# Kernel optimization log

Hardware: AMD Instinct MI355X
Metric: run time of the kernel (lower is better)

## Reference

```python
import math
import jax, jax.numpy as jnp
import numpy as np

B, T, S, D, H, L, DFF, IN, PERIOD = 16, 600, 600, 1024, 8, 8, 4096, 52, 25
HD = D // H
NEG = -1e9


def _param(key, name, shape, scale=0.02):
    k = jax.random.fold_in(key, hash(name) % (2**31))
    return jax.random.normal(k, shape, dtype=jnp.float32) * scale


def setup_inputs() -> dict:
    key = jax.random.key(0)
    k1, k2, k3 = jax.random.split(key, 3)
    inp = {}
    inp["x"] = jax.random.normal(k1, (B, T, IN), dtype=jnp.float32)
    inp["memory"] = jax.random.normal(k2, (B, S, D), dtype=jnp.float32)
    inp["timesteps"] = jax.random.randint(k3, (B,), 0, 1000, dtype=jnp.int32)

    # Periodic positional encoding buffer: sinusoidal over one period, tiled.
    pos = jnp.arange(PERIOD, dtype=jnp.float32)[:, None]
    div = jnp.exp(jnp.arange(0, D, 2, dtype=jnp.float32) * (-math.log(10000.0) / D))
    pe_p = jnp.zeros((PERIOD, D), dtype=jnp.float32)
    pe_p = pe_p.at[:, 0::2].set(jnp.sin(pos * div)).at[:, 1::2].set(jnp.cos(pos * div))
    inp["pe"] = jnp.tile(pe_p, (T // PERIOD + 1, 1))[:T]  # [T, D]

    # ALiBi-style periodic bias (vectorized form of init_bi_biased_mask_faceformer).
    # alibi[h,i,j] = -slope_h * floor((i-j)/period) for j<=i, -slope_h*floor((j-i-1)/period) for j>i
    slopes = jnp.array([0.5 ** (h + 1) for h in range(H)], dtype=jnp.float32)
    di = jnp.arange(T)[:, None] - jnp.arange(T)[None, :]
    steps = jnp.where(di >= 0, di // PERIOD, (-di - 1) // PERIOD).astype(jnp.float32)
    inp["alibi"] = -slopes[:, None, None] * steps[None]  # [H, T, T]

    # Parameters
    inp["W_in"] = _param(key, "W_in", (D, IN))
    inp["b_in"] = jnp.zeros((D,), jnp.float32)
    inp["te_W1"] = _param(key, "te_W1", (D, D))
    inp["te_b1"] = jnp.zeros((D,), jnp.float32)
    inp["te_W2"] = _param(key, "te_W2", (D, D))
    inp["te_b2"] = jnp.zeros((D,), jnp.float32)
    for nm, shape in [
        ("sa_Wqkv", (L, 3 * D, D)), ("sa_bqkv", (L, 3 * D)),
        ("sa_Wo", (L, D, D)), ("sa_bo", (L, D)),
        ("ca_Wqkv", (L, 3 * D, D)), ("ca_bqkv", (L, 3 * D)),
        ("ca_Wo", (L, D, D)), ("ca_bo", (L, D)),
        ("ff_W1", (L, DFF, D)), ("ff_b1", (L, DFF)),
        ("ff_W2", (L, D, DFF)), ("ff_b2", (L, D)),
    ]:
        inp[nm] = _param(key, nm, shape)
    for nm in ["ln1_g", "ln2_g", "ln3_g"]:
        inp[nm] = jnp.ones((L, D), jnp.float32)
    for nm in ["ln1_b", "ln2_b", "ln3_b"]:
        inp[nm] = jnp.zeros((L, D), jnp.float32)
    inp["W_out"] = _param(key, "W_out", (IN, D))
    inp["b_out"] = jnp.zeros((IN,), jnp.float32)
    return inp


def _ln(x, g, b, eps=1e-5):
    mu = jnp.mean(x, axis=-1, keepdims=True)
    var = jnp.mean(jnp.square(x - mu), axis=-1, keepdims=True)
    return (x - mu) * jax.lax.rsqrt(var + eps) * g + b


def _mha(q_in, kv_in, Wqkv, bqkv, Wo, bo, bias):
    # q_in: [B,Tq,D]; kv_in: [B,Tk,D]; bias broadcastable to [B,H,Tq,Tk]
    Wq, Wk, Wv = jnp.split(Wqkv, 3, axis=0)
    bq, bk, bv = jnp.split(bqkv, 3, axis=0)
    Bn, Tq, _ = q_in.shape
    Tk = kv_in.shape[1]
    q = (q_in @ Wq.T + bq).reshape(Bn, Tq, H, HD).transpose(0, 2, 1, 3)
    k = (kv_in @ Wk.T + bk).reshape(Bn, Tk, H, HD).transpose(0, 2, 1, 3)
    v = (kv_in @ Wv.T + bv).reshape(Bn, Tk, H, HD).transpose(0, 2, 1, 3)
    scores = jnp.einsum("bhqd,bhkd->bhqk", q, k) / math.sqrt(HD) + bias
    attn = jax.nn.softmax(scores, axis=-1)
    out = jnp.einsum("bhqk,bhkd->bhqd", attn, v)
    out = out.transpose(0, 2, 1, 3).reshape(Bn, Tq, D)
    return out @ Wo.T + bo


def reference(x, memory, timesteps, pe, alibi, W_in, b_in, te_W1, te_b1, te_W2, te_b2,
              sa_Wqkv, sa_bqkv, sa_Wo, sa_bo, ca_Wqkv, ca_bqkv, ca_Wo, ca_bo,
              ff_W1, ff_b1, ff_W2, ff_b2, ln1_g, ln1_b, ln2_g, ln2_b, ln3_g, ln3_b,
              W_out, b_out):
    # --- timestep embedding (DDPM sinusoidal + 2-layer SiLU MLP) ---
    half = D // 2
    exponent = jnp.exp(-math.log(10000.0) * jnp.arange(half, dtype=jnp.float32) / (half - 1.0))
    emb = timesteps.astype(jnp.float32)[:, None] * exponent[None, :]
    t_emb = jnp.concatenate([jnp.sin(emb), jnp.cos(emb)], axis=-1)  # [B, D]
    t_emb = jax.nn.silu(t_emb @ te_W1.T + te_b1) @ te_W2.T + te_b2
    adapter = t_emb[:, None, :]  # [B, 1, D] adapter token

    # --- input projection + periodic positional encoding ---
    h = x @ W_in.T + b_in + pe[None]  # [B, T, D]

    # --- attention biases (adapter column is always attendable => zero bias) ---
    sa_bias = jnp.concatenate([jnp.zeros((H, T, 1), jnp.float32), alibi], axis=-1)[None]  # [1,H,T,1+T]
    eye = jnp.eye(T, S, dtype=jnp.float32)
    mem_bias = jnp.where(eye > 0, 0.0, NEG)  # FaceFormer diagonal-only memory mask
    mem_bias = jnp.concatenate([jnp.zeros((T, 1), jnp.float32), mem_bias], axis=-1)[None, None]  # [1,1,T,1+S]

    # --- stacked decoder layers (post-norm, adapter prepended to K/V) ---
    for l in range(L):
        x_adpt = jnp.concatenate([adapter, h], axis=1)  # [B, 1+T, D]
        h = _ln(h + _mha(h, x_adpt, sa_Wqkv[l], sa_bqkv[l], sa_Wo[l], sa_bo[l], sa_bias), ln1_g[l], ln1_b[l])
        mem_adpt = jnp.concatenate([adapter, memory], axis=1)  # [B, 1+S, D]
        h = _ln(h + _mha(h, mem_adpt, ca_Wqkv[l], ca_bqkv[l], ca_Wo[l], ca_bo[l], mem_bias), ln2_g[l], ln2_b[l])
        ff = jax.nn.relu(h @ ff_W1[l].T + ff_b1[l]) @ ff_W2[l].T + ff_b2[l]
        h = _ln(h + ff, ln3_g[l], ln3_b[l])

    return h @ W_out.T + b_out  # [B, T, IN]
```

## Files before the change

kernel.cpp:

```cpp
#include <hip/hip_runtime.h>
#include <stdint.h>

#define B_ 16
#define T_ 600
#define S_ 600
#define D_ 1024
#define H_ 8
#define HD_ 128
#define L_ 8
#define DFF_ 4096
#define IN_ 52
#define TP1 601
#define MTOK 9600
#define MPAD 9728
#define VTK 608

typedef unsigned short u16;
typedef float f32x4 __attribute__((ext_vector_type(4)));
typedef __bf16 bf16x8 __attribute__((ext_vector_type(8)));

__device__ __forceinline__ u16 f2bf(float f){
  union { float f; unsigned u; } v; v.f = f;
  v.u += 0x7FFFu + ((v.u >> 16) & 1u);
  return (u16)(v.u >> 16);
}
__device__ __forceinline__ float bf2f(u16 h){
  union { unsigned u; float f; } v; v.u = ((unsigned)h) << 16;
  return v.f;
}
__device__ __forceinline__ void gld_lds16(const void* g, void* l){
  __builtin_amdgcn_global_load_lds(
      (const __attribute__((address_space(1))) void*)(uintptr_t)g,
      (__attribute__((address_space(3))) void*)(uintptr_t)l, 16, 0, 0);
}
__device__ __forceinline__ f32x4 MM(bf16x8 a, bf16x8 b, f32x4 c){
  return __builtin_amdgcn_mfma_f32_16x16x32_bf16(a, b, c, 0, 0, 0);
}
#define BAR() asm volatile("s_barrier" ::: "memory")

template<int EPI>
__global__ __launch_bounds__(512, 2)
void k_gemm256(const u16* __restrict__ A, const u16* __restrict__ W,
               const float* __restrict__ bias, void* __restrict__ Cout,
               float* __restrict__ hres, int N, int K, int Mstore){
  __shared__ u16 lds[65536];
  const int t = threadIdx.x;
  const int w = t >> 6, l = t & 63;
  const int lr = l & 15, lg = l >> 4;
  const int wr = w >> 2, wc = w & 3;

  int lin = blockIdx.y * gridDim.x + blockIdx.x;
  const int nwg = gridDim.x * gridDim.y;
  lin = (lin & 7) * (nwg >> 3) + (lin >> 3);
  const long m0 = (long)(lin / gridDim.x) * 256;
  const long n0 = (long)(lin % gridDim.x) * 256;

  const int srow = w*8 + (l >> 3);
  const int schk = (l & 7) ^ (l >> 3);
  const u16* gA = A + (m0 + srow) * (long)K + schk * 8;
  const u16* gB = W + (n0 + srow) * (long)K + schk * 8;

  const int chk0 = ((    lg) ^ (lr & 7)) * 8;
  const int chk1 = ((4 + lg) ^ (lr & 7)) * 8;
  const int arow = (wr*128 + lr) * 64;
  const int brow = (wc*64  + lr) * 64 + 16384;

  f32x4 acc[8][4] = {};
  const int NT = K >> 6;

#define STG_A(i) gld_lds16(gA + (long)(i)*64*K + nc, (void*)(lds + nb + (i)*4096 + w*512))
#define STG_B(i) gld_lds16(gB + (long)(i)*64*K + nc, (void*)(lds + nb + 16384 + (i)*4096 + w*512))
#define LOADF(mq, CH) \
    a0 = *(const bf16x8*)(lds + bufo + arow + ((mq)*4+0)*1024 + (CH)); \
    a1 = *(const bf16x8*)(lds + bufo + arow + ((mq)*4+1)*1024 + (CH)); \
    a2 = *(const bf16x8*)(lds + bufo + arow + ((mq)*4+2)*1024 + (CH)); \
    a3 = *(const bf16x8*)(lds + bufo + arow + ((mq)*4+3)*1024 + (CH)); \
    b0 = *(const bf16x8*)(lds + bufo + brow + 0*1024 + (CH)); \
    b1 = *(const bf16x8*)(lds + bufo + brow + 1*1024 + (CH)); \
    b2 = *(const bf16x8*)(lds + bufo + brow + 2*1024 + (CH));  \
    b3 = *(const bf16x8*)(lds + bufo + brow + 3*1024 + (CH));
#define MFMA16(mq) \
    __builtin_amdgcn_s_setprio(1); \
    { const bf16x8 aa[4] = {a0,a1,a2,a3}; const bf16x8 bb4[4] = {b0,b1,b2,b3}; \
      _Pragma("unroll") for (int i_ = 0; i_ < 4; i_++) \
        _Pragma("unroll") for (int j_ = 0; j_ < 4; j_++) \
          acc[(mq)*4+i_][j_] = MM(aa[i_], bb4[j_], acc[(mq)*4+i_][j_]); } \
    __builtin_amdgcn_s_setprio(0);

  { const int nb = 0; const long nc = 0;
    STG_B(0); STG_B(1); STG_B(2); STG_B(3);
    STG_A(0); STG_A(2); STG_A(1); STG_A(3);
  }
  asm volatile("s_waitcnt vmcnt(2)" ::: "memory");
  BAR();

  int bufo = 0;
  for (int tt = 0; tt < NT; ++tt){
    const int nb = bufo ^ 32768;
    const bool st = (tt + 1 < NT);
    const long nc = (long)(tt + 1) * 64;
    bf16x8 a0,a1,a2,a3,b0,b1,b2,b3;
    LOADF(0, chk0);
    if (st){ STG_B(0); STG_B(1); }
    BAR();
    MFMA16(0);
    BAR();
    LOADF(0, chk1);
    if (st){ STG_B(2); STG_B(3); asm volatile("s_waitcnt vmcnt(4)" ::: "memory"); }
    else   {                     asm volatile("s_waitcnt vmcnt(0)" ::: "memory"); }
    BAR();
    MFMA16(0);
    BAR();
    LOADF(1, chk0);
    if (st){ STG_A(0); STG_A(2); }
    BAR();
    MFMA16(1);
    BAR();
    LOADF(1, chk1);
    if (st){ STG_A(1); STG_A(3); asm volatile("s_waitcnt vmcnt(2)" ::: "memory"); }
    BAR();
    MFMA16(1);
    BAR();
    bufo = nb;
  }
#undef STG_A
#undef STG_B
#undef LOADF
#undef MFMA16

  const int r4 = lg * 4;
#pragma unroll
  for (int nf = 0; nf < 4; nf++){
    const long col = n0 + wc*64 + nf*16 + lr;
    const float bv = bias[col];
#pragma unroll
    for (int mf = 0; mf < 8; mf++){
      const long row = m0 + wr*128 + mf*16 + r4;
      if (EPI == 2 && row >= Mstore) continue;
#pragma unroll
      for (int r = 0; r < 4; r++){
        float v = acc[mf][nf][r] + bv;
        if (EPI == 1) v = fmaxf(v, 0.f);
        if (EPI == 2) hres[(row + r) * (long)N + col] += v;
        else          ((u16*)Cout)[(row + r) * (long)N + col] = f2bf(v);
      }
    }
  }
}

template<int EPI>
__global__ __launch_bounds__(512, 4)
void k_gemm_n64(const u16* __restrict__ A, const u16* __restrict__ W,
                const float* __restrict__ bias, void* __restrict__ Cout,
                float* __restrict__ hres, int N, int K, int Mstore){
  __shared__ u16 lds[40960];
  const int t = threadIdx.x;
  const int w = t >> 6, l = t & 63;
  const int lr = l & 15, lg = l >> 4;
  const int wr = w >> 1, wcc = w & 1;

  int lin = blockIdx.y * gridDim.x + blockIdx.x;
  const int nwg = gridDim.x * gridDim.y;
  lin = (lin & 7) * (nwg >> 3) + (lin >> 3);
  const long m0 = (long)(lin / gridDim.x) * 256;
  const long n0 = (long)(lin % gridDim.x) * 64;

  const int srow = w*8 + (l >> 3);
  const int schk = (l & 7) ^ (l >> 3);
  const u16* gA = A + (m0 + srow) * (long)K + schk * 8;
  const u16* gB = W + (n0 + srow) * (long)K + schk * 8;

  const int swz = lr & 7;
  const int arowb = wr*4096 + lr*64;
  const int browb = 16384 + (wcc*32 + lr)*64;

  f32x4 acc[4][2] = {};
  const int NT = K >> 6;

#define STG_A64(i) gld_lds16(gA + (long)(i)*64*K + nc, (void*)(lds + nb + (i)*4096 + w*512))
#define STG_B64()  gld_lds16(gB + nc,                  (void*)(lds + nb + 16384 + w*512))
#define LOADF64(kk) \
    a0 = *(const bf16x8*)(lds + bufo + arowb + 0*1024 + (((kk)*4+lg)^swz)*8); \
    a1 = *(const bf16x8*)(lds + bufo + arowb + 1*1024 + (((kk)*4+lg)^swz)*8); \
    a2 = *(const bf16x8*)(lds + bufo + arowb + 2*1024 + (((kk)*4+lg)^swz)*8); \
    a3 = *(const bf16x8*)(lds + bufo + arowb + 3*1024 + (((kk)*4+lg)^swz)*8); \
    b0 = *(const bf16x8*)(lds + bufo + browb + 0*1024 + (((kk)*4+lg)^swz)*8); \
    b1 = *(const bf16x8*)(lds + bufo + browb + 1*1024 + (((kk)*4+lg)^swz)*8);
#define MFMA8() \
    __builtin_amdgcn_s_setprio(1); \
    { const bf16x8 aa[4] = {a0,a1,a2,a3}; \
      _Pragma("unroll") for (int i_ = 0; i_ < 4; i_++){ \
        acc[i_][0] = MM(aa[i_], b0, acc[i_][0]); \
        acc[i_][1] = MM(aa[i_], b1, acc[i_][1]); } } \
    __builtin_amdgcn_s_setprio(0);

  { const int nb = 0; const long nc = 0;
    STG_B64(); STG_A64(0); STG_A64(1); STG_A64(2); STG_A64(3);
  }
  asm volatile("s_waitcnt vmcnt(0)" ::: "memory");
  BAR();

  int bufo = 0;
  for (int tt = 0; tt < NT; ++tt){
    const int nb = (bufo ^ 20480);
    const bool st = (tt + 1 < NT);
    const long nc = (long)(tt + 1) * 64;
    bf16x8 a0,a1,a2,a3,b0,b1;
    if (st){ STG_B64(); STG_A64(0); STG_A64(1); STG_A64(2); STG_A64(3); }
    LOADF64(0);
    MFMA8();
    LOADF64(1);
    MFMA8();
    if (st) asm volatile("s_waitcnt vmcnt(0)" ::: "memory");
    BAR();
    bufo = nb;
  }
#undef STG_A64
#undef STG_B64
#undef LOADF64
#undef MFMA8

  const int r4 = lg * 4;
#pragma unroll
  for (int nf = 0; nf < 2; nf++){
    const long col = n0 + wcc*32 + nf*16 + lr;
    const float bv = bias[col];
#pragma unroll
    for (int mf = 0; mf < 4; mf++){
      const long row = m0 + wr*64 + mf*16 + r4;
      if (EPI == 2 && row >= Mstore) continue;
#pragma unroll
      for (int r = 0; r < 4; r++){
        float v = acc[mf][nf][r] + bv;
        if (EPI == 1) v = fmaxf(v, 0.f);
        if (EPI == 2) hres[(row + r) * (long)N + col] += v;
        else          ((u16*)Cout)[(row + r) * (long)N + col] = f2bf(v);
      }
    }
  }
}

__global__ __launch_bounds__(256)
void k_gemm_in(const u16* __restrict__ A, const u16* __restrict__ W,
               const float* __restrict__ bias, const float* __restrict__ pe,
               float* __restrict__ hf, u16* __restrict__ hbf){
  __shared__ u16 sA[128*64];
  __shared__ u16 sB[128*64];
  const int t = threadIdx.x;
  const int w = t >> 6, l = t & 63;
  const int lr = l & 15, lg = l >> 4;
  const long m0 = (long)blockIdx.y * 128;
  const long n0 = (long)blockIdx.x * 128;
  const int wm = (w >> 1) << 6, wn = (w & 1) << 6;
  const int srow = t >> 3;
  const int schk = (t & 7) ^ (srow & 7);
  const u16* gA = A + (m0 + srow) * 64 + schk * 8;
  const u16* gB = W + (n0 + srow) * 64 + schk * 8;
#pragma unroll
  for (int i = 0; i < 4; i++){
    gld_lds16(gA + i*32*64, (void*)(sA + i*2048 + (t>>6)*512));
    gld_lds16(gB + i*32*64, (void*)(sB + i*2048 + (t>>6)*512));
  }
  asm volatile("s_waitcnt vmcnt(0)" ::: "memory");
  __syncthreads();
  f32x4 acc[4][4] = {};
#pragma unroll
  for (int kk = 0; kk < 2; kk++){
    bf16x8 af[4], bfv[4];
#pragma unroll
    for (int i = 0; i < 4; i++){
      const int row = wm + i*16 + lr;
      af[i] = *(const bf16x8*)(sA + row*64 + ((kk*4+lg)^(row&7))*8);
    }
#pragma unroll
    for (int j = 0; j < 4; j++){
      const int row = wn + j*16 + lr;
      bfv[j] = *(const bf16x8*)(sB + row*64 + ((kk*4+lg)^(row&7))*8);
    }
#pragma unroll
    for (int i = 0; i < 4; i++)
#pragma unroll
      for (int j = 0; j < 4; j++)
        acc[i][j] = MM(af[i], bfv[j], acc[i][j]);
  }
  const int r0 = lg * 4;
#pragma unroll
  for (int j = 0; j < 4; j++){
    const long col = n0 + wn + j*16 + lr;
    const float bv = bias[col];
#pragma unroll
    for (int i = 0; i < 4; i++){
      const long row = m0 + wm + i*16 + r0;
#pragma unroll
      for (int r = 0; r < 4; r++){
        const long rr = row + r;
        if (rr >= MTOK) continue;
        const float v = acc[i][j][r] + bv + pe[(rr % 25)*1024 + col];
        hf[rr*1024 + col] = v;
        hbf[rr*1024 + col] = f2bf(v);
      }
    }
  }
}

__global__ __launch_bounds__(256)
void k_gemm_out(const u16* __restrict__ A, const u16* __restrict__ W,
                const float* __restrict__ bias, float* __restrict__ outp){
  __shared__ u16 sA[128*32];
  __shared__ u16 sB[128*32];
  const int t = threadIdx.x;
  const int w = t >> 6, l = t & 63;
  const long m0 = (long)blockIdx.y * 128;
  const int wm = (w >> 1) << 6, wn = (w & 1) << 6;
  const int K = 1024;
  f32x4 acc[4][4] = {};
  const char* gA0 = (const char*)(A + (m0 + (t >> 2)) * (long)K) + (t & 3) * 16;
  const char* gA1 = gA0 + 64 * (long)K * 2;
  const char* gB0 = (const char*)(W + (long)(t >> 2) * K) + (t & 3) * 16;
  const char* gB1 = gB0 + 64 * (long)K * 2;
  char* lA = (char*)sA + w * 1024;
  char* lB = (char*)sB + w * 1024;
  const int lr = l & 15;
  const int lkb = (l >> 4) * 16;
  for (long k0 = 0; k0 < K; k0 += 32){
    const long kb = k0 * 2;
    gld_lds16(gA0 + kb, lA);
    gld_lds16(gA1 + kb, lA + 4096);
    gld_lds16(gB0 + kb, lB);
    gld_lds16(gB1 + kb, lB + 4096);
    __syncthreads();
    bf16x8 af[4], bfv[4];
#pragma unroll
    for (int i = 0; i < 4; i++)
      af[i] = *(const bf16x8*)((const char*)sA + (wm + i*16 + lr)*64 + lkb);
#pragma unroll
    for (int j = 0; j < 4; j++)
      bfv[j] = *(const bf16x8*)((const char*)sB + (wn + j*16 + lr)*64 + lkb);
#pragma unroll
    for (int i = 0; i < 4; i++)
#pragma unroll
      for (int j = 0; j < 4; j++)
        acc[i][j] = MM(af[i], bfv[j], acc[i][j]);
    __syncthreads();
  }
  const int r0 = (l >> 4) * 4;
#pragma unroll
  for (int j = 0; j < 4; j++){
    const int col = wn + j*16 + lr;
    if (col >= IN_) continue;
    const float bv = bias[col];
#pragma unroll
    for (int i = 0; i < 4; i++){
      const long row = m0 + wm + i*16 + r0;
#pragma unroll
      for (int r = 0; r < 4; r++)
        outp[(row + r) * (long)IN_ + col] = acc[i][j][r] + bv;
    }
  }
}

__global__ __launch_bounds__(256)
void k_vtrans(const u16* __restrict__ qkv, u16* __restrict__ vt){
  const int b = blockIdx.z;
  const int h = blockIdx.y >> 1;
  const int d0 = (blockIdx.y & 1) * 64;
  const int k0 = blockIdx.x * 64;
  __shared__ u16 tile[64][72];
  const int t = threadIdx.x;
#pragma unroll
  for (int it = 0; it < 2; it++){
    const int idx = t + it*256;
    const int kk = idx >> 3;
    const int dd = (idx & 7) * 8;
    const int kabs = k0 + kk;
    union { bf16x8 v; u16 us[8]; } u;
    if (kabs <= 600)
      u.v = *(const bf16x8*)(qkv + ((long)b*TP1 + kabs)*3072 + 2048 + h*128 + d0 + dd);
    else {
#pragma unroll
      for (int j = 0; j < 8; j++) u.us[j] = 0;
    }
    *(bf16x8*)(&tile[kk][dd]) = u.v;
  }
  __syncthreads();
#pragma unroll
  for (int it = 0; it < 2; it++){
    const int idx = t + it*256;
    const int dd = idx >> 3;
    const int kc = (idx & 7) * 8;
    if (k0 + kc + 7 < VTK){
      union { uint4 o; u16 us[8]; } u;
#pragma unroll
      for (int j = 0; j < 8; j++) u.us[j] = tile[kc + j][dd];
      *(uint4*)(vt + ((long)(b*8 + h)*128 + d0 + dd)*VTK + k0 + kc) = u.o;
    }
  }
}

__global__ __launch_bounds__(256)
void k_sa_attn3(const u16* __restrict__ qkv, const u16* __restrict__ vt,
                u16* __restrict__ outp){
  const int id = blockIdx.x;
  const int g  = id & 127;
  const int qt = id >> 7;
  const int b = g >> 3, h = g & 7;
  const int w = threadIdx.x >> 6, l = threadIdx.x & 63;
  const int lr = l & 15, lg = l >> 4;
  const int q0 = qt * 64 + w * 16;
  const float scale = 0.08838834764831845f;
  const float slope = exp2f(-(float)(h + 1));

  __shared__ u16 Kl[2][4096];
  __shared__ u16 Vl[2][4096];
  __shared__ u16 Pl[4][16*32];
  __shared__ float cS[4][16];
  __shared__ float iS[4][16];

  const long bb = (long)b * TP1;
  const u16* qptr = qkv + (bb + 1 + q0 + lr) * 3072 + h * 128 + lg * 8;
  bf16x8 aq[4];
#pragma unroll
  for (int kk = 0; kk < 4; kk++) aq[kk] = *(const bf16x8*)(qptr + kk * 32);

  const int kj0 = w*2, kj1 = w*2 + 1;
  const int kkey0 = kj0*4 + (l >> 4), kkey1 = kj1*4 + (l >> 4);
  const u16* kg0 = qkv + (bb + kkey0)*3072 + 1024 + h*128 + (((l&15) ^ (kkey0&7)))*8;
  const u16* kg1 = qkv + (bb + kkey1)*3072 + 1024 + h*128 + (((l&15) ^ (kkey1&7)))*8;
  const u16* vbase = vt + (long)(b*8 + h) * 128 * VTK;
  const int vd0 = kj0*16 + (l >> 2), vd1 = kj1*16 + (l >> 2);
  const u16* vg0 = vbase + (long)vd0*VTK + ((l&3) ^ (vd0&3))*8;
  const u16* vg1 = vbase + (long)vd1*VTK + ((l&3) ^ (vd1&3))*8;

#define STAGE(buf, kb) \
  gld_lds16(kg0 + (long)(kb)*3072, (void*)(Kl[buf] + kj0*512)); \
  gld_lds16(kg1 + (long)(kb)*3072, (void*)(Kl[buf] + kj1*512)); \
  gld_lds16(vg0 + (kb),            (void*)(Vl[buf] + kj0*512)); \
  gld_lds16(vg1 + (kb),            (void*)(Vl[buf] + kj1*512));

  f32x4 o[8] = {};
  float mrow[4] = {-1e30f, -1e30f, -1e30f, -1e30f};
  float lsum[4] = {0.f, 0.f, 0.f, 0.f};

  STAGE(0, 0);
  asm volatile("s_waitcnt vmcnt(0)" ::: "memory");
  BAR();

  for (int kt = 0; kt < 19; kt++){
    const int kb0 = kt * 32;
    const int cur = kt & 1;
    const bool st = (kt < 18);
    if (st){ STAGE(cur ^ 1, kb0 + 32); }
    f32x4 s0 = {}, s1 = {};
#pragma unroll
    for (int kk = 0; kk < 4; kk++){
      const int sw = ((kk*4 + lg) ^ (lr & 7)) * 8;
      bf16x8 bk0 = *(const bf16x8*)(Kl[cur] + lr*128 + sw);
      bf16x8 bk1 = *(const bf16x8*)(Kl[cur] + (lr+16)*128 + sw);
      s0 = MM(aq[kk], bk0, s0);
      s1 = MM(aq[kk], bk1, s1);
    }
#pragma unroll
    for (int r = 0; r < 4; r++){
      const int iq = q0 + lg * 4 + r;
      float v0 = s0[r] * scale, v1 = s1[r] * scale;
      const int k0a = kb0 + lr, k1a = kb0 + 16 + lr;
      if (k0a >= 601) v0 = -1e30f;
      else if (k0a > 0){
        const int j = k0a - 1, di = iq - j;
        const int st2 = di >= 0 ? di/25 : (-di-1)/25;
        v0 -= slope * (float)st2;
      }
      if (k1a >= 601) v1 = -1e30f;
      else {
        const int j = k1a - 1, di = iq - j;
        const int st2 = di >= 0 ? di/25 : (-di-1)/25;
        v1 -= slope * (float)st2;
      }
      float mx = fmaxf(v0, v1);
#pragma unroll
      for (int d = 8; d >= 1; d >>= 1) mx = fmaxf(mx, __shfl_xor(mx, d, 64));
      const float mnew = fmaxf(mrow[r], mx);
      const float corr = __expf(mrow[r] - mnew);
      const float p0 = __expf(v0 - mnew);
      const float p1 = __expf(v1 - mnew);
      float rs = p0 + p1;
#pragma unroll
      for (int d = 8; d >= 1; d >>= 1) rs += __shfl_xor(rs, d, 64);
      lsum[r] = lsum[r] * corr + rs;
      mrow[r] = mnew;
      if (lr == 0) cS[w][lg*4 + r] = corr;
      Pl[w][(lg*4 + r)*32 + lr]      = f2bf(p0);
      Pl[w][(lg*4 + r)*32 + 16 + lr] = f2bf(p1);
    }
    const float c = cS[w][lr];
    const bool resc = __any(c != 1.0f);
    const bf16x8 pa = *(const bf16x8*)(&Pl[w][lr*32 + lg*8]);
#pragma unroll
    for (int dc = 0; dc < 8; dc++){
      const int d = dc*16 + lr;
      const bf16x8 va = *(const bf16x8*)(Vl[cur] + d*32 + ((lg ^ (d & 3))*8));
      if (resc){
#pragma unroll
        for (int rr = 0; rr < 4; rr++) o[dc][rr] *= c;
      }
      o[dc] = MM(va, pa, o[dc]);
    }
    if (st){
      asm volatile("s_waitcnt vmcnt(0)" ::: "memory");
      BAR();
    }
  }
#undef STAGE
#pragma unroll
  for (int r = 0; r < 4; r++)
    if (lr == 0) iS[w][lg*4 + r] = 1.f / lsum[r];
  const int tq = q0 + lr;
  if (tq < 600){
    const float inv = iS[w][lr];
    u16* op = outp + ((long)b*600 + tq) * 1024 + h * 128;
#pragma unroll
    for (int dc = 0; dc < 8; dc++){
      union { uint2 o8; u16 us[4]; } pk;
#pragma unroll
      for (int rr = 0; rr < 4; rr++) pk.us[rr] = f2bf(o[dc][rr] * inv);
      *(uint2*)(op + dc*16 + lg*4) = pk.o8;
    }
  }
}

__global__ __launch_bounds__(256)
void k_ca_attn(const u16* __restrict__ qca, const u16* __restrict__ kv,
               u16* __restrict__ outp){
  const int wid = blockIdx.x * 4 + (threadIdx.x >> 6);
  const int l = threadIdx.x & 63;
  if (wid >= MTOK) return;
  const int b = wid / 600, t = wid % 600;
  const u16* q  = qca + (long)wid * 1024;
  const u16* ka = kv + ((long)b * TP1) * 2048;
  const u16* km = kv + ((long)(b * TP1 + 1 + t)) * 2048;
  const float scale = 0.08838834764831845f;
#pragma unroll
  for (int h = 0; h < 8; h++){
    const int d = h*128 + l*2;
    const float q0 = bf2f(q[d]),  q1 = bf2f(q[d+1]);
    float s0 = q0*bf2f(ka[d]) + q1*bf2f(ka[d+1]);
    float s1 = q0*bf2f(km[d]) + q1*bf2f(km[d+1]);
#pragma unroll
    for (int dd = 32; dd >= 1; dd >>= 1){
      s0 += __shfl_xor(s0, dd, 64);
      s1 += __shfl_xor(s1, dd, 64);
    }
    s0 *= scale; s1 *= scale;
    const float mx = fmaxf(s0, s1);
    const float e0 = __expf(s0 - mx), e1 = __expf(s1 - mx);
    const float inv = 1.f / (e0 + e1);
    const float o0 = (e0*bf2f(ka[1024+d])   + e1*bf2f(km[1024+d]))   * inv;
    const float o1 = (e0*bf2f(ka[1024+d+1]) + e1*bf2f(km[1024+d+1])) * inv;
    const unsigned pack = (unsigned)f2bf(o0) | ((unsigned)f2bf(o1) << 16);
    *(unsigned*)(outp + (long)wid*1024 + d) = pack;
  }
}

__global__ __launch_bounds__(256)
void k_ln2(float* __restrict__ hf, const float* __restrict__ g,
           const float* __restrict__ bb, u16* __restrict__ hbf){
  const long m = blockIdx.x;
  float* r = hf + m*1024;
  float vals[4];
  float sum = 0.f, sumsq = 0.f;
#pragma unroll
  for (int i = 0; i < 4; i++){
    const int idx = threadIdx.x + i*256;
    const float v = r[idx];
    vals[i] = v; sum += v; sumsq += v*v;
  }
#pragma unroll
  for (int d = 32; d >= 1; d >>= 1){ sum += __shfl_xor(sum,d,64); sumsq += __shfl_xor(sumsq,d,64); }
  __shared__ float red[8];
  const int w = threadIdx.x >> 6;
  if ((threadIdx.x & 63) == 0){ red[w] = sum; red[4+w] = sumsq; }
  __syncthreads();
  sum   = red[0]+red[1]+red[2]+red[3];
  sumsq = red[4]+red[5]+red[6]+red[7];
  const float mu  = sum * (1.f/1024.f);
  const float var = sumsq * (1.f/1024.f) - mu*mu;
  const float rstd = rsqrtf(var + 1e-5f);
#pragma unroll
  for (int i = 0; i < 4; i++){
    const int idx = threadIdx.x + i*256;
    const float y = (vals[i] - mu) * rstd * g[idx] + bb[idx];
    r[idx] = y;
    hbf[m*1024+idx] = f2bf(y);
  }
}

__global__ void k_temb_sin(const int* __restrict__ ts, float* __restrict__ emb){
  const int b = blockIdx.x;
  const float t = (float)ts[b];
  for (int j = threadIdx.x; j < 1024; j += 256){
    const int jj = j < 512 ? j : j - 512;
    const float ex = expf(-9.210340371976184f * (float)jj / 511.0f);
    const float v = t * ex;
    emb[b*1024 + j] = (j < 512) ? sinf(v) : cosf(v);
  }
}

__global__ void k_te_mm(const float* __restrict__ in, const float* __restrict__ W,
                        const float* __restrict__ bv, float* __restrict__ outp,
                        int act, u16* __restrict__ xad, u16* __restrict__ mad){
  __shared__ float row[1024];
  const int b = blockIdx.y;
  for (int k = threadIdx.x; k < 1024; k += 256) row[k] = in[b*1024 + k];
  __syncthreads();
  const int n = blockIdx.x*256 + threadIdx.x;
  const float* wr = W + (long)n*1024;
  float s = 0.f;
  for (int k = 0; k < 1024; k += 4){
    const float4 w4 = *(const float4*)(wr + k);
    s += row[k]*w4.x + row[k+1]*w4.y + row[k+2]*w4.z + row[k+3]*w4.w;
  }
  s += bv[n];
  if (act) s = s / (1.f + expf(-s));
  outp[b*1024 + n] = s;
  if (xad){
    const u16 h = f2bf(s);
    xad[((long)b*TP1)*1024 + n] = h;
    mad[((long)b*TP1)*1024 + n] = h;
  }
}

__global__ void k_convert_weights(const float* __restrict__ sqkv, const float* __restrict__ swo,
                                  const float* __restrict__ cqkv, const float* __restrict__ cwo,
                                  const float* __restrict__ fw1,  const float* __restrict__ fw2,
                                  u16* __restrict__ wbuf){
  const long idx = ((long)blockIdx.x*256 + threadIdx.x) * 8;
  const float* src; long off;
  if      (idx <  3145728L){ src = sqkv; off = idx; }
  else if (idx <  4194304L){ src = swo;  off = idx -  3145728L; }
  else if (idx <  7340032L){ src = cqkv; off = idx -  4194304L; }
  else if (idx <  8388608L){ src = cwo;  off = idx -  7340032L; }
  else if (idx < 12582912L){ src = fw1;  off = idx -  8388608L; }
  else                     { src = fw2;  off = idx - 12582912L; }
  const float4 a = *(const float4*)(src + off);
  const float4 c = *(const float4*)(src + off + 4);
  uint4 o;
  o.x = (unsigned)f2bf(a.x) | ((unsigned)f2bf(a.y) << 16);
  o.y = (unsigned)f2bf(a.z) | ((unsigned)f2bf(a.w) << 16);
  o.z = (unsigned)f2bf(c.x) | ((unsigned)f2bf(c.y) << 16);
  o.w = (unsigned)f2bf(c.z) | ((unsigned)f2bf(c.w) << 16);
  *(uint4*)(wbuf + idx) = o;
}

__global__ void k_convert_wout(const float* __restrict__ src, u16* __restrict__ dst){
  const int i = blockIdx.x*256 + threadIdx.x;
  const int row = i >> 10;
  dst[i] = (row < IN_) ? f2bf(src[i]) : (u16)0;
}

__global__ void k_convert_x(const float* __restrict__ x, u16* __restrict__ dst){
  const int i = blockIdx.x*256 + threadIdx.x;
  const int row = i >> 6, c = i & 63;
  float v = 0.f;
  if (row < MTOK && c < IN_) v = x[(long)row*IN_ + c];
  dst[i] = f2bf(v);
}

__global__ void k_convert_win(const float* __restrict__ wi, u16* __restrict__ dst){
  const int i = blockIdx.x*256 + threadIdx.x;
  const int row = i >> 6, c = i & 63;
  dst[i] = (c < IN_) ? f2bf(wi[(long)row*IN_ + c]) : (u16)0;
}

__global__ void k_build_memadpt(const float* __restrict__ mem, u16* __restrict__ mad){
  const long i = ((long)blockIdx.x*256 + threadIdx.x) * 8;
  const long tok = i >> 10, col = i & 1023;
  const long b = tok / 600, s = tok % 600;
  const float4 a = *(const float4*)(mem + i);
  const float4 c = *(const float4*)(mem + i + 4);
  uint4 o;
  o.x = (unsigned)f2bf(a.x) | ((unsigned)f2bf(a.y) << 16);
  o.y = (unsigned)f2bf(a.z) | ((unsigned)f2bf(a.w) << 16);
  o.z = (unsigned)f2bf(c.x) | ((unsigned)f2bf(c.y) << 16);
  o.w = (unsigned)f2bf(c.z) | ((unsigned)f2bf(c.w) << 16);
  *(uint4*)(mad + ((b*TP1 + 1 + s) << 10) + col) = o;
}

__global__ void k_h_to_xadpt(const u16* __restrict__ hbf, u16* __restrict__ xad){
  const long i = ((long)blockIdx.x*256 + threadIdx.x) * 8;
  const long tok = i >> 10, col = i & 1023;
  const long b = tok / 600, t = tok % 600;
  *(uint4*)(xad + ((b*TP1 + 1 + t) << 10) + col) = *(const uint4*)(hbf + i);
}

extern "C" void kernel_launch(void* const* d_in, const int* in_sizes, int n_in,
                              void* d_out, int out_size, void* d_ws, size_t ws_size,
                              hipStream_t stream){
  const float* x        = (const float*)d_in[0];
  const float* memory   = (const float*)d_in[1];
  const int*   tsteps   = (const int*)  d_in[2];
  const float* pe       = (const float*)d_in[3];
  const float* W_in     = (const float*)d_in[5];
  const float* b_in     = (const float*)d_in[6];
  const float* te_W1    = (const float*)d_in[7];
  const float* te_b1    = (const float*)d_in[8];
  const float* te_W2    = (const float*)d_in[9];
  const float* te_b2    = (const float*)d_in[10];
  const float* sa_Wqkv  = (const float*)d_in[11];
  const float* sa_bqkv  = (const float*)d_in[12];
  const float* sa_Wo    = (const float*)d_in[13];
  const float* sa_bo    = (const float*)d_in[14];
  const float* ca_Wqkv  = (const float*)d_in[15];
  const float* ca_bqkv  = (const float*)d_in[16];
  const float* ca_Wo    = (const float*)d_in[17];
  const float* ca_bo    = (const float*)d_in[18];
  const float* ff_W1    = (const float*)d_in[19];
  const float* ff_b1    = (const float*)d_in[20];
  const float* ff_W2    = (const float*)d_in[21];
  const float* ff_b2    = (const float*)d_in[22];
  const float* ln1_g    = (const float*)d_in[23];
  const float* ln2_g    = (const float*)d_in[24];
  const float* ln3_g    = (const float*)d_in[25];
  const float* ln1_b    = (const float*)d_in[26];
  const float* ln2_b    = (const float*)d_in[27];
  const float* ln3_b    = (const float*)d_in[28];
  const float* W_out    = (const float*)d_in[29];
  const float* b_out    = (const float*)d_in[30];

  char* ws = (char*)d_ws;
  float* h_f    = (float*)(ws + 0);
  u16*   h_bf   = (u16*)  (ws + 39321600);
  u16*   attn_bf= (u16*)  (ws + 58982400);
  u16*   xadpt  = (u16*)  (ws + 78643200);
  u16*   madpt  = (u16*)  (ws + 98336768);
  u16*   qkv    = (u16*)  (ws + 118030336);
  u16*   ffb    = (u16*)  (ws + 177799168);
  u16*   wbuf   = (u16*)  (ws + 257490944);
  float* temb_a = (float*)(ws + 177799168);
  float* temb_b = (float*)(ws + 177864704);
  u16*   vtg    = (u16*)  (ws + 177799168 + 262144);
  u16*   x_bf   = wbuf;
  u16*   win_bf = wbuf + 622592;
  u16*   wout_bf= wbuf;

  u16* qca  = qkv;
  u16* kvca = qkv + (long)MPAD * 1024;

  k_temb_sin<<<dim3(16), dim3(256), 0, stream>>>(tsteps, temb_a);
  k_te_mm<<<dim3(4,16), dim3(256), 0, stream>>>(temb_a, te_W1, te_b1, temb_b, 1, (u16*)nullptr, (u16*)nullptr);
  k_te_mm<<<dim3(4,16), dim3(256), 0, stream>>>(temb_b, te_W2, te_b2, temb_a, 0, xadpt, madpt);
  k_build_memadpt<<<dim3(4800), dim3(256), 0, stream>>>(memory, madpt);
  k_convert_x<<<dim3(2432), dim3(256), 0, stream>>>(x, x_bf);
  k_convert_win<<<dim3(256), dim3(256), 0, stream>>>(W_in, win_bf);
  k_gemm_in<<<dim3(8,76), dim3(256), 0, stream>>>(x_bf, win_bf, b_in, pe, h_f, h_bf);

  for (int l = 0; l < L_; l++){
    k_convert_weights<<<dim3(8192), dim3(256), 0, stream>>>(
        sa_Wqkv + (long)l*3145728, sa_Wo + (long)l*1048576,
        ca_Wqkv + (long)l*3145728, ca_Wo + (long)l*1048576,
        ff_W1 + (long)l*4194304,  ff_W2 + (long)l*4194304, wbuf);
    k_h_to_xadpt<<<dim3(4800), dim3(256), 0, stream>>>(h_bf, xadpt);
    k_gemm256<0><<<dim3(12,38), dim3(512), 0, stream>>>(xadpt, wbuf, sa_bqkv + l*3072, (void*)qkv, h_f, 3072, 1024, MPAD);
    k_vtrans<<<dim3(10,16,16), dim3(256), 0, stream>>>(qkv, vtg);
    k_sa_attn3<<<dim3(1280), dim3(256), 0, stream>>>(qkv, vtg, attn_bf);
    k_gemm_n64<2><<<dim3(16,38), dim3(512), 0, stream>>>(attn_bf, wbuf + 3145728, sa_bo + l*1024, nullptr, h_f, 1024, 1024, MTOK);
    k_ln2<<<dim3(9600), dim3(256), 0, stream>>>(h_f, ln1_g + l*1024, ln1_b + l*1024, h_bf);
    k_gemm_n64<0><<<dim3(16,38), dim3(512), 0, stream>>>(h_bf, wbuf + 4194304, ca_bqkv + l*3072, (void*)qca, h_f, 1024, 1024, MPAD);
    k_gemm_n64<0><<<dim3(32,38), dim3(512), 0, stream>>>(madpt, wbuf + 4194304 + 1048576, ca_bqkv + l*3072 + 1024, (void*)kvca, h_f, 2048, 1024, MPAD);
    k_ca_attn<<<dim3(2400), dim3(256), 0, stream>>>(qca, kvca, attn_bf);
    k_gemm_n64<2><<<dim3(16,38), dim3(512), 0, stream>>>(attn_bf, wbuf + 7340032, ca_bo + l*1024, nullptr, h_f, 1024, 1024, MTOK);
    k_ln2<<<dim3(9600), dim3(256), 0, stream>>>(h_f, ln2_g + l*1024, ln2_b + l*1024, h_bf);
    k_gemm256<1><<<dim3(16,38), dim3(512), 0, stream>>>(h_bf, wbuf + 8388608, ff_b1 + l*4096, (void*)ffb, h_f, 4096, 1024, MPAD);
    k_gemm_n64<2><<<dim3(16,38), dim3(512), 0, stream>>>(ffb, wbuf + 12582912, ff_b2 + l*1024, nullptr, h_f, 1024, 4096, MTOK);
    k_ln2<<<dim3(9600), dim3(256), 0, stream>>>(h_f, ln3_g + l*1024, ln3_b + l*1024, h_bf);
  }
  k_convert_wout<<<dim3(512), dim3(256), 0, stream>>>(W_out, wout_bf);
  k_gemm_out<<<dim3(1,75), dim3(256), 0, stream>>>(h_bf, wout_bf, b_out, (float*)d_out);
}
```

Measured before the change: 5.885 ms.

## Restructure n64 GEMM warp tiling with split-phase loads; fuse adapter copy into LN

The N=64 GEMM changes its warp layout from 4x2 warps (64x32 each) to 2x4 warps (128x16 each). Its main loop now has two halves with partial vmcnt waits and an extra barrier, so global-to-LDS staging of the next tile overlaps the MFMAs. The launch bound drops to 2 blocks per SM, which gives the compiler more registers but may lower occupancy. Separately, the k_h_to_xadpt copy kernel is removed: the input GEMM and the last LayerNorm of each layer now write the bf16 hidden state straight into the adapter-prefixed buffer, saving one launch and one read/write pass per layer.

```diff
diff --git a/kernel.cpp b/kernel.cpp
--- a/kernel.cpp
+++ b/kernel.cpp
@@ -149,7 +149,7 @@
 }
 
 template<int EPI>
-__global__ __launch_bounds__(512, 4)
+__global__ __launch_bounds__(512, 2)
 void k_gemm_n64(const u16* __restrict__ A, const u16* __restrict__ W,
                 const float* __restrict__ bias, void* __restrict__ Cout,
                 float* __restrict__ hres, int N, int K, int Mstore){
@@ -157,7 +157,7 @@
   const int t = threadIdx.x;
   const int w = t >> 6, l = t & 63;
   const int lr = l & 15, lg = l >> 4;
-  const int wr = w >> 1, wcc = w & 1;
+  const int wr2 = w >> 2, wc4 = w & 3;
 
   int lin = blockIdx.y * gridDim.x + blockIdx.x;
   const int nwg = gridDim.x * gridDim.y;
@@ -171,33 +171,20 @@
   const u16* gB = W + (n0 + srow) * (long)K + schk * 8;
 
   const int swz = lr & 7;
-  const int arowb = wr*4096 + lr*64;
-  const int browb = 16384 + (wcc*32 + lr)*64;
-
-  f32x4 acc[4][2] = {};
+  const int arow_lo = wr2*8192 + lr*64;
+  const int arow_hi = arow_lo + 4096;
+  const int browb   = 16384 + (wc4*16 + lr)*64;
+
+  f32x4 acc[8] = {};
   const int NT = K >> 6;
 
 #define STG_A64(i) gld_lds16(gA + (long)(i)*64*K + nc, (void*)(lds + nb + (i)*4096 + w*512))
 #define STG_B64()  gld_lds16(gB + nc,                  (void*)(lds + nb + 16384 + w*512))
-#define LOADF64(kk) \
-    a0 = *(const bf16x8*)(lds + bufo + arowb + 0*1024 + (((kk)*4+lg)^swz)*8); \
-    a1 = *(const bf16x8*)(lds + bufo + arowb + 1*1024 + (((kk)*4+lg)^swz)*8); \
-    a2 = *(const bf16x8*)(lds + bufo + arowb + 2*1024 + (((kk)*4+lg)^swz)*8); \
-    a3 = *(const bf16x8*)(lds + bufo + arowb + 3*1024 + (((kk)*4+lg)^swz)*8); \
-    b0 = *(const bf16x8*)(lds + bufo + browb + 0*1024 + (((kk)*4+lg)^swz)*8); \
-    b1 = *(const bf16x8*)(lds + bufo + browb + 1*1024 + (((kk)*4+lg)^swz)*8);
-#define MFMA8() \
-    __builtin_amdgcn_s_setprio(1); \
-    { const bf16x8 aa[4] = {a0,a1,a2,a3}; \
-      _Pragma("unroll") for (int i_ = 0; i_ < 4; i_++){ \
-        acc[i_][0] = MM(aa[i_], b0, acc[i_][0]); \
-        acc[i_][1] = MM(aa[i_], b1, acc[i_][1]); } } \
-    __builtin_amdgcn_s_setprio(0);
 
   { const int nb = 0; const long nc = 0;
-    STG_B64(); STG_A64(0); STG_A64(1); STG_A64(2); STG_A64(3);
-  }
-  asm volatile("s_waitcnt vmcnt(0)" ::: "memory");
+    STG_B64(); STG_A64(0); STG_A64(2); STG_A64(1); STG_A64(3);
+  }
+  asm volatile("s_waitcnt vmcnt(2)" ::: "memory");
   BAR();
 
   int bufo = 0;
@@ -205,37 +192,64 @@
     const int nb = (bufo ^ 20480);
     const bool st = (tt + 1 < NT);
     const long nc = (long)(tt + 1) * 64;
-    bf16x8 a0,a1,a2,a3,b0,b1;
-    if (st){ STG_B64(); STG_A64(0); STG_A64(1); STG_A64(2); STG_A64(3); }
-    LOADF64(0);
-    MFMA8();
-    LOADF64(1);
-    MFMA8();
-    if (st) asm volatile("s_waitcnt vmcnt(0)" ::: "memory");
+    const int c0 = (lg ^ swz) * 8;
+    const int c1 = ((4 + lg) ^ swz) * 8;
+    bf16x8 a00,a10,a20,a30,a01,a11,a21,a31,b0,b1;
+    b0  = *(const bf16x8*)(lds + bufo + browb + c0);
+    b1  = *(const bf16x8*)(lds + bufo + browb + c1);
+    a00 = *(const bf16x8*)(lds + bufo + arow_lo + 0*1024 + c0);
+    a10 = *(const bf16x8*)(lds + bufo + arow_lo + 1*1024 + c0);
+    a20 = *(const bf16x8*)(lds + bufo + arow_lo + 2*1024 + c0);
+    a30 = *(const bf16x8*)(lds + bufo + arow_lo + 3*1024 + c0);
+    a01 = *(const bf16x8*)(lds + bufo + arow_lo + 0*1024 + c1);
+    a11 = *(const bf16x8*)(lds + bufo + arow_lo + 1*1024 + c1);
+    a21 = *(const bf16x8*)(lds + bufo + arow_lo + 2*1024 + c1);
+    a31 = *(const bf16x8*)(lds + bufo + arow_lo + 3*1024 + c1);
+    if (st){ STG_B64(); STG_A64(0); STG_A64(2); }
+    __builtin_amdgcn_s_setprio(1);
+    acc[0] = MM(a00, b0, acc[0]); acc[0] = MM(a01, b1, acc[0]);
+    acc[1] = MM(a10, b0, acc[1]); acc[1] = MM(a11, b1, acc[1]);
+    acc[2] = MM(a20, b0, acc[2]); acc[2] = MM(a21, b1, acc[2]);
+    acc[3] = MM(a30, b0, acc[3]); acc[3] = MM(a31, b1, acc[3]);
+    __builtin_amdgcn_s_setprio(0);
+    if (st) asm volatile("s_waitcnt vmcnt(3)" ::: "memory");
+    else    asm volatile("s_waitcnt vmcnt(0)" ::: "memory");
+    BAR();
+    a00 = *(const bf16x8*)(lds + bufo + arow_hi + 0*1024 + c0);
+    a10 = *(const bf16x8*)(lds + bufo + arow_hi + 1*1024 + c0);
+    a20 = *(const bf16x8*)(lds + bufo + arow_hi + 2*1024 + c0);
+    a30 = *(const bf16x8*)(lds + bufo + arow_hi + 3*1024 + c0);
+    a01 = *(const bf16x8*)(lds + bufo + arow_hi + 0*1024 + c1);
+    a11 = *(const bf16x8*)(lds + bufo + arow_hi + 1*1024 + c1);
+    a21 = *(const bf16x8*)(lds + bufo + arow_hi + 2*1024 + c1);
+    a31 = *(const bf16x8*)(lds + bufo + arow_hi + 3*1024 + c1);
+    if (st){ STG_A64(1); STG_A64(3); }
+    __builtin_amdgcn_s_setprio(1);
+    acc[4] = MM(a00, b0, acc[4]); acc[4] = MM(a01, b1, acc[4]);
+    acc[5] = MM(a10, b0, acc[5]); acc[5] = MM(a11, b1, acc[5]);
+    acc[6] = MM(a20, b0, acc[6]); acc[6] = MM(a21, b1, acc[6]);
+    acc[7] = MM(a30, b0, acc[7]); acc[7] = MM(a31, b1, acc[7]);
+    __builtin_amdgcn_s_setprio(0);
+    if (st) asm volatile("s_waitcnt vmcnt(2)" ::: "memory");
     BAR();
     bufo = nb;
   }
 #undef STG_A64
 #undef STG_B64
-#undef LOADF64
-#undef MFMA8
 
   const int r4 = lg * 4;
-#pragma unroll
-  for (int nf = 0; nf < 2; nf++){
-    const long col = n0 + wcc*32 + nf*16 + lr;
-    const float bv = bias[col];
-#pragma unroll
-    for (int mf = 0; mf < 4; mf++){
-      const long row = m0 + wr*64 + mf*16 + r4;
-      if (EPI == 2 && row >= Mstore) continue;
-#pragma unroll
-      for (int r = 0; r < 4; r++){
-        float v = acc[mf][nf][r] + bv;
-        if (EPI == 1) v = fmaxf(v, 0.f);
-        if (EPI == 2) hres[(row + r) * (long)N + col] += v;
-        else          ((u16*)Cout)[(row + r) * (long)N + col] = f2bf(v);
-      }
+  const long col = n0 + wc4*16 + lr;
+  const float bv = bias[col];
+#pragma unroll
+  for (int mf = 0; mf < 8; mf++){
+    const long row = m0 + wr2*128 + mf*16 + r4;
+    if (EPI == 2 && row >= Mstore) continue;
+#pragma unroll
+    for (int r = 0; r < 4; r++){
+      float v = acc[mf][r] + bv;
+      if (EPI == 1) v = fmaxf(v, 0.f);
+      if (EPI == 2) hres[(row + r) * (long)N + col] += v;
+      else          ((u16*)Cout)[(row + r) * (long)N + col] = f2bf(v);
     }
   }
 }
@@ -243,7 +257,7 @@
 __global__ __launch_bounds__(256)
 void k_gemm_in(const u16* __restrict__ A, const u16* __restrict__ W,
                const float* __restrict__ bias, const float* __restrict__ pe,
-               float* __restrict__ hf, u16* __restrict__ hbf){
+               float* __restrict__ hf, u16* __restrict__ hbf, u16* __restrict__ xad){
   __shared__ u16 sA[128*64];
   __shared__ u16 sB[128*64];
   const int t = threadIdx.x;
@@ -296,8 +310,11 @@
         const long rr = row + r;
         if (rr >= MTOK) continue;
         const float v = acc[i][j][r] + bv + pe[(rr % 25)*1024 + col];
+        const u16 hv = f2bf(v);
         hf[rr*1024 + col] = v;
-        hbf[rr*1024 + col] = f2bf(v);
+        hbf[rr*1024 + col] = hv;
+        const long bq = rr / 600, tq = rr % 600;
+        xad[((bq*TP1 + 1 + tq) << 10) + col] = hv;
       }
     }
   }
@@ -563,7 +580,8 @@
 
 __global__ __launch_bounds__(256)
 void k_ln2(float* __restrict__ hf, const float* __restrict__ g,
-           const float* __restrict__ bb, u16* __restrict__ hbf){
+           const float* __restrict__ bb, u16* __restrict__ hbf,
+           u16* __restrict__ xad){
   const long m = blockIdx.x;
   float* r = hf + m*1024;
   float vals[4];
@@ -585,12 +603,19 @@
   const float mu  = sum * (1.f/1024.f);
   const float var = sumsq * (1.f/1024.f) - mu*mu;
   const float rstd = rsqrtf(var + 1e-5f);
+  u16* xrow = nullptr;
+  if (xad){
+    const long bq = m / 600, tq = m % 600;
+    xrow = xad + ((bq*TP1 + 1 + tq) << 10);
+  }
 #pragma unroll
   for (int i = 0; i < 4; i++){
     const int idx = threadIdx.x + i*256;
     const float y = (vals[i] - mu) * rstd * g[idx] + bb[idx];
+    const u16 hv = f2bf(y);
     r[idx] = y;
-    hbf[m*1024+idx] = f2bf(y);
+    hbf[m*1024+idx] = hv;
+    if (xad) xrow[idx] = hv;
   }
 }
 
@@ -683,13 +708,6 @@
   o.z = (unsigned)f2bf(c.x) | ((unsigned)f2bf(c.y) << 16);
   o.w = (unsigned)f2bf(c.z) | ((unsigned)f2bf(c.w) << 16);
   *(uint4*)(mad + ((b*TP1 + 1 + s) << 10) + col) = o;
-}
-
-__global__ void k_h_to_xadpt(const u16* __restrict__ hbf, u16* __restrict__ xad){
-  const long i = ((long)blockIdx.x*256 + threadIdx.x) * 8;
-  const long tok = i >> 10, col = i & 1023;
-  const long b = tok / 600, t = tok % 600;
-  *(uint4*)(xad + ((b*TP1 + 1 + t) << 10) + col) = *(const uint4*)(hbf + i);
 }
 
 extern "C" void kernel_launch(void* const* d_in, const int* in_sizes, int n_in,
@@ -751,27 +769,26 @@
   k_build_memadpt<<<dim3(4800), dim3(256), 0, stream>>>(memory, madpt);
   k_convert_x<<<dim3(2432), dim3(256), 0, stream>>>(x, x_bf);
   k_convert_win<<<dim3(256), dim3(256), 0, stream>>>(W_in, win_bf);
-  k_gemm_in<<<dim3(8,76), dim3(256), 0, stream>>>(x_bf, win_bf, b_in, pe, h_f, h_bf);
+  k_gemm_in<<<dim3(8,76), dim3(256), 0, stream>>>(x_bf, win_bf, b_in, pe, h_f, h_bf, xadpt);
 
   for (int l = 0; l < L_; l++){
     k_convert_weights<<<dim3(8192), dim3(256), 0, stream>>>(
         sa_Wqkv + (long)l*3145728, sa_Wo + (long)l*1048576,
         ca_Wqkv + (long)l*3145728, ca_Wo + (long)l*1048576,
         ff_W1 + (long)l*4194304,  ff_W2 + (long)l*4194304, wbuf);
-    k_h_to_xadpt<<<dim3(4800), dim3(256), 0, stream>>>(h_bf, xadpt);
     k_gemm256<0><<<dim3(12,38), dim3(512), 0, stream>>>(xadpt, wbuf, sa_bqkv + l*3072, (void*)qkv, h_f, 3072, 1024, MPAD);
     k_vtrans<<<dim3(10,16,16), dim3(256), 0, stream>>>(qkv, vtg);
     k_sa_attn3<<<dim3(1280), dim3(256), 0, stream>>>(qkv, vtg, attn_bf);
     k_gemm_n64<2><<<dim3(16,38), dim3(512), 0, stream>>>(attn_bf, wbuf + 3145728, sa_bo + l*1024, nullptr, h_f, 1024, 1024, MTOK);
-    k_ln2<<<dim3(9600), dim3(256), 0, stream>>>(h_f, ln1_g + l*1024, ln1_b + l*1024, h_bf);
+    k_ln2<<<dim3(9600), dim3(256), 0, stream>>>(h_f, ln1_g + l*1024, ln1_b + l*1024, h_bf, (u16*)nullptr);
     k_gemm_n64<0><<<dim3(16,38), dim3(512), 0, stream>>>(h_bf, wbuf + 4194304, ca_bqkv + l*3072, (void*)qca, h_f, 1024, 1024, MPAD);
     k_gemm_n64<0><<<dim3(32,38), dim3(512), 0, stream>>>(madpt, wbuf + 4194304 + 1048576, ca_bqkv + l*3072 + 1024, (void*)kvca, h_f, 2048, 1024, MPAD);
     k_ca_attn<<<dim3(2400), dim3(256), 0, stream>>>(qca, kvca, attn_bf);
     k_gemm_n64<2><<<dim3(16,38), dim3(512), 0, stream>>>(attn_bf, wbuf + 7340032, ca_bo + l*1024, nullptr, h_f, 1024, 1024, MTOK);
-    k_ln2<<<dim3(9600), dim3(256), 0, stream>>>(h_f, ln2_g + l*1024, ln2_b + l*1024, h_bf);
+    k_ln2<<<dim3(9600), dim3(256), 0, stream>>>(h_f, ln2_g + l*1024, ln2_b + l*1024, h_bf, (u16*)nullptr);
     k_gemm256<1><<<dim3(16,38), dim3(512), 0, stream>>>(h_bf, wbuf + 8388608, ff_b1 + l*4096, (void*)ffb, h_f, 4096, 1024, MPAD);
     k_gemm_n64<2><<<dim3(16,38), dim3(512), 0, stream>>>(ffb, wbuf + 12582912, ff_b2 + l*1024, nullptr, h_f, 1024, 4096, MTOK);
-    k_ln2<<<dim3(9600), dim3(256), 0, stream>>>(h_f, ln3_g + l*1024, ln3_b + l*1024, h_bf);
+    k_ln2<<<dim3(9600), dim3(256), 0, stream>>>(h_f, ln3_g + l*1024, ln3_b + l*1024, h_bf, xadpt);
   }
   k_convert_wout<<<dim3(512), dim3(256), 0, stream>>>(W_out, wout_bf);
   k_gemm_out<<<dim3(1,75), dim3(256), 0, stream>>>(h_bf, wout_bf, b_out, (float*)d_out);
```

Result: no change. 5.863 ms (-0.4%).
